# Optimization experiments

Hardware: AMD Instinct MI355X
Metric: run time of the kernel (lower is better)

The kernel has to match this reference:

```python
import jax, jax.numpy as jnp
import numpy as np

BS, L, D, N, K = 2048, 100, 256, 16, 32
M_CONST = 2
NEG = -1e9


def setup_inputs() -> dict:
    key = jax.random.key(0)
    ks = jax.random.split(key, 6)
    hist = jax.random.normal(ks[0], (BS, L, D), dtype=jnp.float32)
    hist_mask = jnp.ones((BS, L), dtype=jnp.float32)  # passed but unused by PolyAttention (faithful)
    cand = jax.random.normal(ks[1], (BS, N, D), dtype=jnp.float32)
    num_interests = jax.random.randint(ks[2], (BS,), 1, K + 1, dtype=jnp.int32)
    cat_counts = jax.random.randint(ks[3], (BS,), 1, 21, dtype=jnp.int32)
    W_poly = jax.random.normal(ks[4], (D, D), dtype=jnp.float32) * (1.0 / np.sqrt(D))
    context_codes = jax.random.normal(ks[5], (K, D), dtype=jnp.float32) * (1.0 / np.sqrt(D))
    return {
        "history_news_representations": hist,
        "history_mask": hist_mask,
        "candidate_news_representations": cand,
        "num_extracted_interests": num_interests,
        "unique_category_counts": cat_counts,
        "W_poly": W_poly,
        "context_codes": context_codes,
    }


def _forward(hist, hist_mask, cand, num_interests, cat_counts, W_poly, context_codes):
    # --- PolyAttention ---
    proj = jnp.tanh(jnp.einsum("bld,ed->ble", hist, W_poly))        # [bs, L, ccd]
    weights = jnp.einsum("ble,ke->bkl", proj, context_codes)         # [bs, K, L]
    cc_mask = jnp.arange(K)[None, :] < num_interests[:, None]        # [bs, K]
    weights = jnp.where(cc_mask[:, :, None], weights, NEG)
    weights = jax.nn.softmax(weights, axis=2)
    weights = jnp.nan_to_num(weights, nan=0.0, posinf=0.0, neginf=0.0)
    interests = jnp.einsum("bkl,bld->bkd", weights, hist)            # [bs, K, d]

    # --- InterestCandidateAttention over all N candidates at once ---
    aw = jnp.einsum("bkd,bnd->bnk", interests, cand)                 # [bs, N, K]
    dyn_K = jnp.ceil(jnp.log2(M_CONST * cat_counts.astype(jnp.float32))).astype(jnp.int32)
    dyn_K = jnp.clip(dyn_K, 1, K)                                    # [bs]
    # rank of each entry in descending order along K
    order = jnp.argsort(-aw, axis=-1)
    rank = jnp.argsort(order, axis=-1)                               # [bs, N, K]
    topk_mask = (rank < dyn_K[:, None, None]).astype(aw.dtype)
    masked = aw * topk_mask
    user = jnp.einsum("bnk,bkd->bnd", masked, interests)             # [bs, N, d]
    return user


def reference(history_news_representations, history_mask, candidate_news_representations,
              num_extracted_interests, unique_category_counts, W_poly, context_codes):
    return _forward(history_news_representations, history_mask, candidate_news_representations,
                    num_extracted_interests, unique_category_counts, W_poly, context_codes)
```

## Files before the change

kernel.cpp:

```cpp
#include <hip/hip_runtime.h>
#include <math.h>

#define NEGV (-1e9f)

typedef _Float16 half8 __attribute__((ext_vector_type(8)));
typedef _Float16 half4 __attribute__((ext_vector_type(4)));
typedef float f32x4 __attribute__((ext_vector_type(4)));


__device__ inline float tanh_fast(float x) {
    float t = __expf(2.0f * x);
    float r = __builtin_amdgcn_rcpf(t + 1.0f);
    return fmaf(-2.0f, r, 1.0f);
}

__device__ inline void split4(const float4 v, half4& h, half4& m) {
    const float* p = (const float*)&v;
    #pragma unroll
    for (int q = 0; q < 4; ++q) {
        float x = p[q];
        _Float16 hi = (_Float16)x;
        float res = x - (float)hi;
        h[q] = hi;
        m[q] = (_Float16)res;
    }
}

__device__ inline void split8(const f32x4 a, const f32x4 b, half8& h, half8& m) {
    #pragma unroll
    for (int q = 0; q < 4; ++q) {
        float x = a[q];
        _Float16 hi = (_Float16)x;
        h[q] = hi; m[q] = (_Float16)(x - (float)hi);
    }
    #pragma unroll
    for (int q = 0; q < 4; ++q) {
        float x = b[q];
        _Float16 hi = (_Float16)x;
        h[4+q] = hi; m[4+q] = (_Float16)(x - (float)hi);
    }
}

__global__ __launch_bounds__(256, 2)
void k_proj_logits(const float* __restrict__ hist, const float* __restrict__ W,
                   const float* __restrict__ cc, float* __restrict__ logits)
{
    __shared__ __align__(16) char smem[49152];
    _Float16* Af = (_Float16*)smem;
    _Float16* Bf = (_Float16*)(smem + 16384);
    float (*Pj)[68] = (float(*)[68])smem;

    const int tid  = threadIdx.x;
    const int lane = tid & 63;
    const int w    = tid >> 6;
    const int wr   = w >> 1, wc = w & 1;
    const int g    = lane >> 4;
    const int r    = lane & 15;
    const size_t rowBase = (size_t)blockIdx.x * 128;

    f32x4 acc[4][8];
    #pragma unroll
    for (int i = 0; i < 4; ++i)
        #pragma unroll
        for (int j = 0; j < 8; ++j) acc[i][j] = (f32x4)(0.0f);

    const int aRow = tid >> 3;
    const int c4   = (tid & 7) * 4;
    const int sg   = c4 >> 3;
    const int sj   = c4 & 7;

    float4 aReg[4], bReg[8];
    #pragma unroll
    for (int s = 0; s < 4; ++s)
        aReg[s] = *(const float4*)&hist[(rowBase + aRow + 32 * s) * 256 + c4];
    #pragma unroll
    for (int p = 0; p < 8; ++p)
        bReg[p] = *(const float4*)&W[(size_t)((tid >> 3) + 32 * p) * 256 + c4];

    for (int kt = 0; kt < 256; kt += 32) {
        __syncthreads();
        #pragma unroll
        for (int s = 0; s < 4; ++s) {
            int row = aRow + 32 * s;
            half4 h, m;
            split4(aReg[s], h, m);
            int base = (row >> 4) * 512 + sg * 128 + (row & 15) * 8 + sj;
            *(half4*)&Af[base]        = h;
            *(half4*)&Af[4096 + base] = m;
        }
        #pragma unroll
        for (int p = 0; p < 8; ++p) {
            int e = (tid >> 3) + 32 * p;
            half4 h, m;
            split4(bReg[p], h, m);
            int base = (e >> 4) * 512 + sg * 128 + (e & 15) * 8 + sj;
            *(half4*)&Bf[base]        = h;
            *(half4*)&Bf[8192 + base] = m;
        }
        if (kt < 224) {
            #pragma unroll
            for (int s = 0; s < 4; ++s)
                aReg[s] = *(const float4*)&hist[(rowBase + aRow + 32 * s) * 256 + kt + 32 + c4];
            #pragma unroll
            for (int p = 0; p < 8; ++p)
                bReg[p] = *(const float4*)&W[(size_t)((tid >> 3) + 32 * p) * 256 + kt + 32 + c4];
        }
        __syncthreads();

        half8 Ah[4], Am[4];
        #pragma unroll
        for (int rt = 0; rt < 4; ++rt) {
            int rtg = wr * 4 + rt;
            Ah[rt] = *(half8*)&Af[rtg * 512 + lane * 8];
            Am[rt] = *(half8*)&Af[4096 + rtg * 512 + lane * 8];
        }
        #pragma unroll
        for (int ct = 0; ct < 8; ++ct) {
            int ctg = wc * 8 + ct;
            half8 Bh = *(half8*)&Bf[ctg * 512 + lane * 8];
            half8 Bm = *(half8*)&Bf[8192 + ctg * 512 + lane * 8];
            #pragma unroll
            for (int rt = 0; rt < 4; ++rt) {
                acc[rt][ct] = __builtin_amdgcn_mfma_f32_16x16x32_f16(Ah[rt], Bh, acc[rt][ct], 0, 0, 0);
                acc[rt][ct] = __builtin_amdgcn_mfma_f32_16x16x32_f16(Ah[rt], Bm, acc[rt][ct], 0, 0, 0);
                acc[rt][ct] = __builtin_amdgcn_mfma_f32_16x16x32_f16(Am[rt], Bh, acc[rt][ct], 0, 0, 0);
                acc[rt][ct] = __builtin_amdgcn_mfma_f32_16x16x32_f16(Am[rt], Bm, acc[rt][ct], 0, 0, 0);
            }
        }
    }

    f32x4 acc2[2][2];
    #pragma unroll
    for (int i = 0; i < 2; ++i)
        #pragma unroll
        for (int j = 0; j < 2; ++j) acc2[i][j] = (f32x4)(0.0f);

    #pragma unroll
    for (int ec = 0; ec < 4; ++ec) {
        __syncthreads();
        if (wc == (ec >> 1)) {
            #pragma unroll
            for (int rt = 0; rt < 4; ++rt) {
                #pragma unroll
                for (int c4i = 0; c4i < 4; ++c4i) {
                    int ctm = (ec & 1) * 4 + c4i;
                    f32x4 t = acc[rt][ctm];
                    int el = c4i * 16 + r;
                    int rb = 64 * wr + rt * 16 + g * 4;
                    #pragma unroll
                    for (int i = 0; i < 4; ++i)
                        Pj[rb + i][el] = tanh_fast(t[i]);
                }
            }
        }
        __syncthreads();
        #pragma unroll
        for (int ks = 0; ks < 2; ++ks) {
            half8 Ah2[2], Am2[2];
            #pragma unroll
            for (int rt2 = 0; rt2 < 2; ++rt2) {
                const float* src = &Pj[32 * w + rt2 * 16 + r][ks * 32 + g * 8];
                f32x4 p0 = *(const f32x4*)src;
                f32x4 p1 = *(const f32x4*)(src + 4);
                split8(p0, p1, Ah2[rt2], Am2[rt2]);
            }
            #pragma unroll
            for (int ct = 0; ct < 2; ++ct) {
                const float* csrc = &cc[(size_t)(ct * 16 + r) * 256 + 64 * ec + ks * 32 + g * 8];
                f32x4 q0 = *(const f32x4*)csrc;
                f32x4 q1 = *(const f32x4*)(csrc + 4);
                half8 Bh, Bm;
                split8(q0, q1, Bh, Bm);
                #pragma unroll
                for (int rt2 = 0; rt2 < 2; ++rt2) {
                    acc2[rt2][ct] = __builtin_amdgcn_mfma_f32_16x16x32_f16(Ah2[rt2], Bh, acc2[rt2][ct], 0, 0, 0);
                    acc2[rt2][ct] = __builtin_amdgcn_mfma_f32_16x16x32_f16(Ah2[rt2], Bm, acc2[rt2][ct], 0, 0, 0);
                    acc2[rt2][ct] = __builtin_amdgcn_mfma_f32_16x16x32_f16(Am2[rt2], Bh, acc2[rt2][ct], 0, 0, 0);
                    acc2[rt2][ct] = __builtin_amdgcn_mfma_f32_16x16x32_f16(Am2[rt2], Bm, acc2[rt2][ct], 0, 0, 0);
                }
            }
        }
    }
    #pragma unroll
    for (int rt2 = 0; rt2 < 2; ++rt2)
        #pragma unroll
        for (int ct = 0; ct < 2; ++ct)
            #pragma unroll
            for (int i = 0; i < 4; ++i) {
                size_t grow = rowBase + 32 * w + rt2 * 16 + g * 4 + i;
                logits[grow * 32 + ct * 16 + r] = acc2[rt2][ct][i];
            }
}

__global__ __launch_bounds__(256, 2)
void k_attn(const float* __restrict__ hist, const float* __restrict__ cand,
            const int* __restrict__ numi, const int* __restrict__ catc,
            const float* __restrict__ logits, float* __restrict__ out)
{
    __shared__ float wT[100][36];
    __shared__ float ints[32][260];
    __shared__ float cands[16][260];
    __shared__ float aws[16][36];
    __shared__ float maw[16][36];

    const int tid = threadIdx.x;
    const int b = blockIdx.x;
    const int num = numi[b];

    for (int idx = tid; idx < 3200; idx += 256) {
        int l = idx >> 5;
        int k = idx & 31;
        wT[l][k] = logits[(size_t)b * 3200 + idx];
    }
    #pragma unroll
    for (int s = 0; s < 4; ++s) {
        int idx = tid + s * 256;
        int n = idx >> 6;
        int c4 = (idx & 63) * 4;
        *(float4*)&cands[n][c4] = *(const float4*)&cand[((size_t)b * 16 + n) * 256 + c4];
    }
    __syncthreads();

    {
        const int k = tid >> 3;
        const int lg = tid & 7;
        const bool valid = k < num;
        float vals[13];
        float m = -INFINITY;
        #pragma unroll
        for (int i = 0; i < 13; ++i) {
            int l = lg + 8 * i;
            if (l < 100) {
                float v = valid ? wT[l][k] : NEGV;
                vals[i] = v;
                m = fmaxf(m, v);
            }
        }
        #pragma unroll
        for (int off = 1; off < 8; off <<= 1)
            m = fmaxf(m, __shfl_xor(m, off, 8));
        float s = 0.0f;
        #pragma unroll
        for (int i = 0; i < 13; ++i) {
            int l = lg + 8 * i;
            if (l < 100) {
                float e = expf(vals[i] - m);
                s += e;
                wT[l][k] = e;
            }
        }
        #pragma unroll
        for (int off = 1; off < 8; off <<= 1)
            s += __shfl_xor(s, off, 8);
        float inv = 1.0f / s;
        #pragma unroll
        for (int i = 0; i < 13; ++i) {
            int l = lg + 8 * i;
            if (l < 100) wT[l][k] *= inv;
        }
    }
    __syncthreads();

    {
        const int d = tid;
        float acc[32];
        #pragma unroll
        for (int k = 0; k < 32; ++k) acc[k] = 0.0f;
        for (int l = 0; l < 100; ++l) {
            float h = hist[((size_t)b * 100 + l) * 256 + d];
            const float4* wrow = (const float4*)wT[l];
            #pragma unroll
            for (int kq = 0; kq < 8; ++kq) {
                float4 w4 = wrow[kq];
                acc[4 * kq + 0] += w4.x * h;
                acc[4 * kq + 1] += w4.y * h;
                acc[4 * kq + 2] += w4.z * h;
                acc[4 * kq + 3] += w4.w * h;
            }
        }
        #pragma unroll
        for (int k = 0; k < 32; ++k) ints[k][d] = acc[k];
    }
    __syncthreads();

    {
        const int k = tid & 31;
        const int n1 = tid >> 5;
        float s1 = 0.0f, s2 = 0.0f;
        const float4* irow = (const float4*)ints[k];
        const float4* c1 = (const float4*)cands[n1];
        const float4* c2 = (const float4*)cands[n1 + 8];
        for (int q = 0; q < 64; ++q) {
            float4 iv = irow[q];
            float4 a = c1[q];
            float4 c = c2[q];
            s1 += iv.x * a.x + iv.y * a.y + iv.z * a.z + iv.w * a.w;
            s2 += iv.x * c.x + iv.y * c.y + iv.z * c.z + iv.w * c.w;
        }
        aws[n1][k] = s1;
        aws[n1 + 8][k] = s2;
    }
    __syncthreads();

    {
        int c = catc[b];
        int dynK = 32 - __clz(2 * c - 1);
        const int k = tid & 31;
        const int n1 = tid >> 5;
        #pragma unroll
        for (int h = 0; h < 2; ++h) {
            int n = n1 + 8 * h;
            float a = aws[n][k];
            int cnt = 0;
            #pragma unroll
            for (int j = 0; j < 32; ++j) {
                float aj = aws[n][j];
                cnt += (aj > a) || (aj == a && j < k);
            }
            maw[n][k] = (cnt < dynK) ? a : 0.0f;
        }
    }
    __syncthreads();

    {
        const int dd = tid & 63;
        const int ng = tid >> 6;
        float4 acc4[4];
        #pragma unroll
        for (int nn = 0; nn < 4; ++nn) { acc4[nn].x = acc4[nn].y = acc4[nn].z = acc4[nn].w = 0.0f; }
        for (int k = 0; k < 32; ++k) {
            float4 iv = *(const float4*)&ints[k][4 * dd];
            #pragma unroll
            for (int nn = 0; nn < 4; ++nn) {
                float m = maw[4 * ng + nn][k];
                acc4[nn].x += m * iv.x;
                acc4[nn].y += m * iv.y;
                acc4[nn].z += m * iv.z;
                acc4[nn].w += m * iv.w;
            }
        }
        #pragma unroll
        for (int nn = 0; nn < 4; ++nn) {
            *(float4*)&out[((size_t)b * 16 + 4 * ng + nn) * 256 + 4 * dd] = acc4[nn];
        }
    }
}

extern "C" void kernel_launch(void* const* d_in, const int* in_sizes, int n_in,
                              void* d_out, int out_size, void* d_ws, size_t ws_size,
                              hipStream_t stream) {
    const float* hist = (const float*)d_in[0];
    const float* cand = (const float*)d_in[2];
    const int*   numi = (const int*)d_in[3];
    const int*   catc = (const int*)d_in[4];
    const float* W    = (const float*)d_in[5];
    const float* cc   = (const float*)d_in[6];
    float* out = (float*)d_out;
    float* logits = (float*)d_ws;

    k_proj_logits<<<1600, 256, 0, stream>>>(hist, W, cc, logits);
    k_attn<<<2048, 256, 0, stream>>>(hist, cand, numi, catc, logits, out);
}
```

Measured before the change: 276.2 us.

## Pre-split W to fp16 pairs, drop lo*lo MFMA, restage hist in attention

A new prep kernel converts W once per call into hi/lo fp16 fragments in MFMA layout, and the projection kernel streams them into LDS with global_load_lds instead of splitting W in every block. The A-tile loads are rearranged to match the fragment layout directly. The lo*lo MFMA term is dropped in both GEMMs, cutting matrix work by a quarter at a small precision cost. The attention kernel now double-buffers hist rows through LDS, reads candidates from global instead of LDS, merges buffers to cut shared memory, and raises the occupancy hint to 3 blocks per SM.

Measured after the change: 257.0 us. 7.0% less time.

```diff
diff --git a/kernel.cpp b/kernel.cpp
--- a/kernel.cpp
+++ b/kernel.cpp
@@ -4,7 +4,6 @@
 #define NEGV (-1e9f)
 
 typedef _Float16 half8 __attribute__((ext_vector_type(8)));
-typedef _Float16 half4 __attribute__((ext_vector_type(4)));
 typedef float f32x4 __attribute__((ext_vector_type(4)));
 
 
@@ -14,35 +13,49 @@
     return fmaf(-2.0f, r, 1.0f);
 }
 
-__device__ inline void split4(const float4 v, half4& h, half4& m) {
-    const float* p = (const float*)&v;
+__device__ inline void split8(const float4 a, const float4 b, half8& h, half8& m) {
+    const float* pa = (const float*)&a;
+    const float* pb = (const float*)&b;
     #pragma unroll
     for (int q = 0; q < 4; ++q) {
-        float x = p[q];
-        _Float16 hi = (_Float16)x;
-        float res = x - (float)hi;
-        h[q] = hi;
-        m[q] = (_Float16)res;
-    }
-}
-
-__device__ inline void split8(const f32x4 a, const f32x4 b, half8& h, half8& m) {
-    #pragma unroll
-    for (int q = 0; q < 4; ++q) {
-        float x = a[q];
+        float x = pa[q];
         _Float16 hi = (_Float16)x;
         h[q] = hi; m[q] = (_Float16)(x - (float)hi);
     }
     #pragma unroll
     for (int q = 0; q < 4; ++q) {
-        float x = b[q];
+        float x = pb[q];
         _Float16 hi = (_Float16)x;
         h[4+q] = hi; m[4+q] = (_Float16)(x - (float)hi);
     }
 }
 
+__device__ inline void gload_lds16(const void* g, void* lds) {
+    __builtin_amdgcn_global_load_lds(
+        (const __attribute__((address_space(1))) unsigned int*)g,
+        (__attribute__((address_space(3))) unsigned int*)lds, 16, 0, 0);
+}
+
+__global__ __launch_bounds__(256)
+void k_prep(const float* __restrict__ W, half8* __restrict__ Wf)
+{
+    int slot = blockIdx.x * 256 + threadIdx.x;
+    int kt = slot >> 10;
+    int ct = (slot >> 6) & 15;
+    int lane = slot & 63;
+    int e = ct * 16 + (lane & 15);
+    int g = lane >> 4;
+    const float* src = &W[(size_t)e * 256 + kt * 32 + g * 8];
+    float4 a = *(const float4*)src;
+    float4 b = *(const float4*)(src + 4);
+    half8 h, m;
+    split8(a, b, h, m);
+    Wf[((kt * 2 + 0) * 16 + ct) * 64 + lane] = h;
+    Wf[((kt * 2 + 1) * 16 + ct) * 64 + lane] = m;
+}
+
 __global__ __launch_bounds__(256, 2)
-void k_proj_logits(const float* __restrict__ hist, const float* __restrict__ W,
+void k_proj_logits(const float* __restrict__ hist, const half8* __restrict__ Wf,
                    const float* __restrict__ cc, float* __restrict__ logits)
 {
     __shared__ __align__(16) char smem[49152];
@@ -64,67 +77,60 @@
         #pragma unroll
         for (int j = 0; j < 8; ++j) acc[i][j] = (f32x4)(0.0f);
 
-    const int aRow = tid >> 3;
-    const int c4   = (tid & 7) * 4;
-    const int sg   = c4 >> 3;
-    const int sj   = c4 & 7;
-
-    float4 aReg[4], bReg[8];
-    #pragma unroll
-    for (int s = 0; s < 4; ++s)
-        aReg[s] = *(const float4*)&hist[(rowBase + aRow + 32 * s) * 256 + c4];
-    #pragma unroll
-    for (int p = 0; p < 8; ++p)
-        bReg[p] = *(const float4*)&W[(size_t)((tid >> 3) + 32 * p) * 256 + c4];
-
-    for (int kt = 0; kt < 256; kt += 32) {
+    const float* aSrc0 = &hist[(rowBase + (size_t)(w    ) * 16 + r) * 256 + g * 8];
+    const float* aSrc1 = &hist[(rowBase + (size_t)(w + 4) * 16 + r) * 256 + g * 8];
+
+    float4 a00 = *(const float4*)aSrc0;
+    float4 a01 = *(const float4*)(aSrc0 + 4);
+    float4 a10 = *(const float4*)aSrc1;
+    float4 a11 = *(const float4*)(aSrc1 + 4);
+
+    for (int kt = 0; kt < 8; ++kt) {
         __syncthreads();
-        #pragma unroll
-        for (int s = 0; s < 4; ++s) {
-            int row = aRow + 32 * s;
-            half4 h, m;
-            split4(aReg[s], h, m);
-            int base = (row >> 4) * 512 + sg * 128 + (row & 15) * 8 + sj;
-            *(half4*)&Af[base]        = h;
-            *(half4*)&Af[4096 + base] = m;
-        }
-        #pragma unroll
-        for (int p = 0; p < 8; ++p) {
-            int e = (tid >> 3) + 32 * p;
-            half4 h, m;
-            split4(bReg[p], h, m);
-            int base = (e >> 4) * 512 + sg * 128 + (e & 15) * 8 + sj;
-            *(half4*)&Bf[base]        = h;
-            *(half4*)&Bf[8192 + base] = m;
-        }
-        if (kt < 224) {
-            #pragma unroll
-            for (int s = 0; s < 4; ++s)
-                aReg[s] = *(const float4*)&hist[(rowBase + aRow + 32 * s) * 256 + kt + 32 + c4];
-            #pragma unroll
-            for (int p = 0; p < 8; ++p)
-                bReg[p] = *(const float4*)&W[(size_t)((tid >> 3) + 32 * p) * 256 + kt + 32 + c4];
+        {
+            const char* wsrc = (const char*)Wf + (size_t)kt * 32768 + tid * 16;
+            char* ldst = smem + 16384 + (tid & 192) * 16;
+            #pragma unroll
+            for (int i = 0; i < 8; ++i)
+                gload_lds16(wsrc + i * 4096, ldst + i * 4096);
+        }
+        {
+            half8 h, m;
+            split8(a00, a01, h, m);
+            int u = w * 64 + lane;
+            *(half8*)&Af[u * 8] = h;
+            *(half8*)&Af[(512 + u) * 8] = m;
+            split8(a10, a11, h, m);
+            u = (w + 4) * 64 + lane;
+            *(half8*)&Af[u * 8] = h;
+            *(half8*)&Af[(512 + u) * 8] = m;
+        }
+        if (kt < 7) {
+            int off = (kt + 1) * 32;
+            a00 = *(const float4*)(aSrc0 + off);
+            a01 = *(const float4*)(aSrc0 + off + 4);
+            a10 = *(const float4*)(aSrc1 + off);
+            a11 = *(const float4*)(aSrc1 + off + 4);
         }
         __syncthreads();
 
         half8 Ah[4], Am[4];
         #pragma unroll
         for (int rt = 0; rt < 4; ++rt) {
-            int rtg = wr * 4 + rt;
-            Ah[rt] = *(half8*)&Af[rtg * 512 + lane * 8];
-            Am[rt] = *(half8*)&Af[4096 + rtg * 512 + lane * 8];
+            int u = (wr * 4 + rt) * 64 + lane;
+            Ah[rt] = *(half8*)&Af[u * 8];
+            Am[rt] = *(half8*)&Af[(512 + u) * 8];
         }
         #pragma unroll
         for (int ct = 0; ct < 8; ++ct) {
             int ctg = wc * 8 + ct;
-            half8 Bh = *(half8*)&Bf[ctg * 512 + lane * 8];
-            half8 Bm = *(half8*)&Bf[8192 + ctg * 512 + lane * 8];
+            half8 Bh = *(half8*)&Bf[(ctg * 64 + lane) * 8];
+            half8 Bm = *(half8*)&Bf[((1024 + ctg * 64 + lane)) * 8];
             #pragma unroll
             for (int rt = 0; rt < 4; ++rt) {
                 acc[rt][ct] = __builtin_amdgcn_mfma_f32_16x16x32_f16(Ah[rt], Bh, acc[rt][ct], 0, 0, 0);
                 acc[rt][ct] = __builtin_amdgcn_mfma_f32_16x16x32_f16(Ah[rt], Bm, acc[rt][ct], 0, 0, 0);
                 acc[rt][ct] = __builtin_amdgcn_mfma_f32_16x16x32_f16(Am[rt], Bh, acc[rt][ct], 0, 0, 0);
-                acc[rt][ct] = __builtin_amdgcn_mfma_f32_16x16x32_f16(Am[rt], Bm, acc[rt][ct], 0, 0, 0);
             }
         }
     }
@@ -160,15 +166,15 @@
             #pragma unroll
             for (int rt2 = 0; rt2 < 2; ++rt2) {
                 const float* src = &Pj[32 * w + rt2 * 16 + r][ks * 32 + g * 8];
-                f32x4 p0 = *(const f32x4*)src;
-                f32x4 p1 = *(const f32x4*)(src + 4);
+                float4 p0 = *(const float4*)src;
+                float4 p1 = *(const float4*)(src + 4);
                 split8(p0, p1, Ah2[rt2], Am2[rt2]);
             }
             #pragma unroll
             for (int ct = 0; ct < 2; ++ct) {
                 const float* csrc = &cc[(size_t)(ct * 16 + r) * 256 + 64 * ec + ks * 32 + g * 8];
-                f32x4 q0 = *(const f32x4*)csrc;
-                f32x4 q1 = *(const f32x4*)(csrc + 4);
+                float4 q0 = *(const float4*)csrc;
+                float4 q1 = *(const float4*)(csrc + 4);
                 half8 Bh, Bm;
                 split8(q0, q1, Bh, Bm);
                 #pragma unroll
@@ -176,7 +182,6 @@
                     acc2[rt2][ct] = __builtin_amdgcn_mfma_f32_16x16x32_f16(Ah2[rt2], Bh, acc2[rt2][ct], 0, 0, 0);
                     acc2[rt2][ct] = __builtin_amdgcn_mfma_f32_16x16x32_f16(Ah2[rt2], Bm, acc2[rt2][ct], 0, 0, 0);
                     acc2[rt2][ct] = __builtin_amdgcn_mfma_f32_16x16x32_f16(Am2[rt2], Bh, acc2[rt2][ct], 0, 0, 0);
-                    acc2[rt2][ct] = __builtin_amdgcn_mfma_f32_16x16x32_f16(Am2[rt2], Bm, acc2[rt2][ct], 0, 0, 0);
                 }
             }
         }
@@ -192,14 +197,13 @@
             }
 }
 
-__global__ __launch_bounds__(256, 2)
+__global__ __launch_bounds__(256, 3)
 void k_attn(const float* __restrict__ hist, const float* __restrict__ cand,
             const int* __restrict__ numi, const int* __restrict__ catc,
             const float* __restrict__ logits, float* __restrict__ out)
 {
     __shared__ float wT[100][36];
-    __shared__ float ints[32][260];
-    __shared__ float cands[16][260];
+    __shared__ float ib[32][260];
     __shared__ float aws[16][36];
     __shared__ float maw[16][36];
 
@@ -211,13 +215,6 @@
         int l = idx >> 5;
         int k = idx & 31;
         wT[l][k] = logits[(size_t)b * 3200 + idx];
-    }
-    #pragma unroll
-    for (int s = 0; s < 4; ++s) {
-        int idx = tid + s * 256;
-        int n = idx >> 6;
-        int c4 = (idx & 63) * 4;
-        *(float4*)&cands[n][c4] = *(const float4*)&cand[((size_t)b * 16 + n) * 256 + c4];
     }
     __syncthreads();
 
@@ -262,43 +259,80 @@
     __syncthreads();
 
     {
-        const int d = tid;
         float acc[32];
         #pragma unroll
         for (int k = 0; k < 32; ++k) acc[k] = 0.0f;
-        for (int l = 0; l < 100; ++l) {
-            float h = hist[((size_t)b * 100 + l) * 256 + d];
-            const float4* wrow = (const float4*)wT[l];
-            #pragma unroll
-            for (int kq = 0; kq < 8; ++kq) {
-                float4 w4 = wrow[kq];
-                acc[4 * kq + 0] += w4.x * h;
-                acc[4 * kq + 1] += w4.y * h;
-                acc[4 * kq + 2] += w4.z * h;
-                acc[4 * kq + 3] += w4.w * h;
-            }
-        }
-        #pragma unroll
-        for (int k = 0; k < 32; ++k) ints[k][d] = acc[k];
+
+        #pragma unroll
+        for (int s = 0; s < 4; ++s) {
+            int idx = tid + s * 256;
+            int lp = idx >> 6;
+            int c4 = (idx & 63) * 4;
+            *(float4*)&ib[lp][c4] = *(const float4*)&hist[((size_t)b * 100 + lp) * 256 + c4];
+        }
+        __syncthreads();
+
+        for (int c = 0; c < 7; ++c) {
+            float4 pre[4];
+            if (c < 6) {
+                #pragma unroll
+                for (int s = 0; s < 4; ++s) {
+                    int idx = tid + s * 256;
+                    int lp = idx >> 6;
+                    int c4 = (idx & 63) * 4;
+                    int l = 16 * (c + 1) + lp;
+                    pre[s] = (l < 100) ? *(const float4*)&hist[((size_t)b * 100 + l) * 256 + c4]
+                                       : float4{0.f, 0.f, 0.f, 0.f};
+                }
+            }
+            int rows = (c == 6) ? 4 : 16;
+            const int rb = (c & 1) * 16;
+            #pragma unroll 4
+            for (int lp = 0; lp < rows; ++lp) {
+                float h = ib[rb + lp][tid];
+                const float4* wrow = (const float4*)wT[16 * c + lp];
+                #pragma unroll
+                for (int kq = 0; kq < 8; ++kq) {
+                    float4 w4 = wrow[kq];
+                    acc[4 * kq + 0] = fmaf(w4.x, h, acc[4 * kq + 0]);
+                    acc[4 * kq + 1] = fmaf(w4.y, h, acc[4 * kq + 1]);
+                    acc[4 * kq + 2] = fmaf(w4.z, h, acc[4 * kq + 2]);
+                    acc[4 * kq + 3] = fmaf(w4.w, h, acc[4 * kq + 3]);
+                }
+            }
+            if (c < 6) {
+                const int wb = ((c + 1) & 1) * 16;
+                #pragma unroll
+                for (int s = 0; s < 4; ++s) {
+                    int idx = tid + s * 256;
+                    int lp = idx >> 6;
+                    int c4 = (idx & 63) * 4;
+                    *(float4*)&ib[wb + lp][c4] = pre[s];
+                }
+            }
+            __syncthreads();
+        }
+        #pragma unroll
+        for (int k = 0; k < 32; ++k) ib[k][tid] = acc[k];
     }
     __syncthreads();
 
     {
-        const int k = tid & 31;
-        const int n1 = tid >> 5;
-        float s1 = 0.0f, s2 = 0.0f;
-        const float4* irow = (const float4*)ints[k];
-        const float4* c1 = (const float4*)cands[n1];
-        const float4* c2 = (const float4*)cands[n1 + 8];
+        const int n = tid & 15;
+        const int kq = tid >> 4;
+        const float4* cg = (const float4*)&cand[((size_t)b * 16 + n) * 256];
+        const float4* i0 = (const float4*)&ib[kq][0];
+        const float4* i1 = (const float4*)&ib[kq + 16][0];
+        float s0 = 0.0f, s1 = 0.0f;
         for (int q = 0; q < 64; ++q) {
-            float4 iv = irow[q];
-            float4 a = c1[q];
-            float4 c = c2[q];
-            s1 += iv.x * a.x + iv.y * a.y + iv.z * a.z + iv.w * a.w;
-            s2 += iv.x * c.x + iv.y * c.y + iv.z * c.z + iv.w * c.w;
-        }
-        aws[n1][k] = s1;
-        aws[n1 + 8][k] = s2;
+            float4 cv = cg[q];
+            float4 a0 = i0[q];
+            float4 a1 = i1[q];
+            s0 += a0.x * cv.x + a0.y * cv.y + a0.z * cv.z + a0.w * cv.w;
+            s1 += a1.x * cv.x + a1.y * cv.y + a1.z * cv.z + a1.w * cv.w;
+        }
+        aws[n][kq] = s0;
+        aws[n][kq + 16] = s1;
     }
     __syncthreads();
 
@@ -329,14 +363,14 @@
         #pragma unroll
         for (int nn = 0; nn < 4; ++nn) { acc4[nn].x = acc4[nn].y = acc4[nn].z = acc4[nn].w = 0.0f; }
         for (int k = 0; k < 32; ++k) {
-            float4 iv = *(const float4*)&ints[k][4 * dd];
+            float4 iv = *(const float4*)&ib[k][4 * dd];
             #pragma unroll
             for (int nn = 0; nn < 4; ++nn) {
                 float m = maw[4 * ng + nn][k];
-                acc4[nn].x += m * iv.x;
-                acc4[nn].y += m * iv.y;
-                acc4[nn].z += m * iv.z;
-                acc4[nn].w += m * iv.w;
+                acc4[nn].x = fmaf(m, iv.x, acc4[nn].x);
+                acc4[nn].y = fmaf(m, iv.y, acc4[nn].y);
+                acc4[nn].z = fmaf(m, iv.z, acc4[nn].z);
+                acc4[nn].w = fmaf(m, iv.w, acc4[nn].w);
             }
         }
         #pragma unroll
@@ -357,7 +391,13 @@
     const float* cc   = (const float*)d_in[6];
     float* out = (float*)d_out;
     float* logits = (float*)d_ws;
-
-    k_proj_logits<<<1600, 256, 0, stream>>>(hist, W, cc, logits);
+    const size_t LOG_BYTES = 26214400;
+    const size_t WF_BYTES = 262144;
+    half8* Wf = (ws_size >= LOG_BYTES + WF_BYTES)
+                ? (half8*)((char*)d_ws + LOG_BYTES)
+                : (half8*)d_out;
+
+    k_prep<<<32, 256, 0, stream>>>(W, Wf);
+    k_proj_logits<<<1600, 256, 0, stream>>>(hist, Wf, cc, logits);
     k_attn<<<2048, 256, 0, stream>>>(hist, cand, numi, catc, logits, out);
 }
```
